# Optimization experiments

Hardware: AMD Instinct MI355X
Metric: run time of the kernel (lower is better)

Reference implementation:

```python
import jax, jax.numpy as jnp
import numpy as np

B, C, N, K, C_OUT = 16, 64, 2048, 3, 64


def setup_inputs() -> dict:
    key = jax.random.key(0)
    k1, k2, k3 = jax.random.split(key, 3)
    x = jax.random.normal(k1, (B, C, N), dtype=jnp.float32)
    # Conv1d params: weight [out_ch, in_ch, K], bias [out_ch]
    fan_in = C * K
    bound = 1.0 / np.sqrt(fan_in)
    W = jax.random.uniform(k2, (C_OUT, C, K), dtype=jnp.float32, minval=-bound, maxval=bound)
    b = jax.random.uniform(k3, (C_OUT,), dtype=jnp.float32, minval=-bound, maxval=bound)
    return {"x": x, "W": W, "b": b}


def reference(x, W, b):
    # x: [B, C, N]
    # pairwise squared-distance matrix over the length dim: [B, N, N]
    norm_sq = jnp.sum(x * x, axis=1, keepdims=True)              # [B, 1, N]
    dot = jnp.einsum('bcn,bcm->bnm', x, x)                       # [B, N, N]
    dist = norm_sq + jnp.swapaxes(norm_sq, 1, 2) - 2.0 * dot     # [B, N, N]
    # K smallest distances per point (self included, dist=0)
    _, idx = jax.lax.top_k(-dist, K)                             # [B, N, K]
    # gather neighbors: prime[b, c, n*K + k] = x[b, c, idx[b, n, k]]
    idx_flat = idx.reshape(B, 1, N * K)
    prime = jnp.take_along_axis(x, jnp.broadcast_to(idx_flat, (B, C, N * K)), axis=2)
    # Conv1d(kernel=K, stride=K, padding=0) -> [B, C_OUT, N]
    out = jax.lax.conv_general_dilated(
        prime, W, window_strides=(K,), padding='VALID',
        dimension_numbers=('NCH', 'OIH', 'NCH'))
    out = out + b[None, :, None]
    return jax.nn.relu(out)
```

## Files before the change

### kernel.cpp

```cpp
#include <hip/hip_runtime.h>
#include <float.h>

#define BB 16
#define CC 64
#define NN 2048
#define KNN 3
#define COUT 64
#define SPL 8

typedef _Float16 half8 __attribute__((ext_vector_type(8)));
typedef float f32x16 __attribute__((ext_vector_type(16)));

union u4h8 { uint4 v; half8 h; };

__device__ __forceinline__ void gl_lds16(const void* g, void* l) {
    __builtin_amdgcn_global_load_lds(
        (const __attribute__((address_space(1))) unsigned*)g,
        (__attribute__((address_space(3))) unsigned*)l, 16, 0, 0);
}

__global__ __launch_bounds__(256) void k_prep(const float* __restrict__ x,
                                              uint4* __restrict__ xe,
                                              unsigned* __restrict__ anc) {
    __shared__ float t[64][65];
    __shared__ float nsh[64];
    const int b = blockIdx.x;
    const int n0 = blockIdx.y * 64;
    const int tid = threadIdx.x;
    const int ln = tid & 63, g = tid >> 6;
#pragma unroll
    for (int i = 0; i < 16; ++i) {
        const int c = g + 4 * i;
        t[c][ln] = x[((size_t)b * CC + c) * NN + n0 + ln];
    }
    __syncthreads();
    if (tid < 64) {
        float s = 0.f;
#pragma unroll
        for (int c = 0; c < 64; ++c) s = fmaf(t[c][tid], t[c][tid], s);
        nsh[tid] = s;
    }
#pragma unroll
    for (int i = 0; i < 4; ++i) {
        const int cid = tid + 256 * i;
        const int lane = cid & 63;
        const int kblk = (cid >> 6) & 7;
        const int ctl = cid >> 9;
        const int m = ctl * 32 + (lane & 31);
        const int khalf = (lane >> 5) * 8;
        union { uint4 v; _Float16 h[8]; } pk;
#pragma unroll
        for (int j = 0; j < 8; ++j) {
            const int kg = kblk * 16 + khalf + j;
            const int ch = kg & 63;
            const float f = t[ch][m];
            const _Float16 hi = (_Float16)f;
            pk.h[j] = (kg < 64) ? hi : (_Float16)(f - (float)hi);
        }
        const int ct = (n0 >> 5) + ctl;
        xe[((size_t)(b * 64 + ct) * 8 + kblk) * 64 + lane] = pk.v;
    }
    __syncthreads();
    if (tid < 64) {
        const int ctl = tid >> 5, l = tid & 31;
        const int ct = (n0 >> 5) + ctl;
        const float h = -0.5f * nsh[ctl * 32 + l];
        const _Float16 a0 = (_Float16)h;
        const _Float16 a1 = (_Float16)(h - (float)a0);
        union { unsigned u; _Float16 hh[2]; } cu;
        cu.hh[0] = a0; cu.hh[1] = a1;
        anc[(size_t)(b * 64 + ct) * 32 + l] = cu.u;
    }
}

__global__ __launch_bounds__(256) void k_wprep(const float* __restrict__ W,
                                               uint4* __restrict__ Wf) {
    const int tid = threadIdx.x;
#pragma unroll
    for (int i = 0; i < 6; ++i) {
        const int id = tid + 256 * i;
        const int l = id & 63;
        const int kb = (id >> 6) & 3;
        const int ct2 = (id >> 8) & 1;
        const int kk = id >> 9;
        const int co = ct2 * 32 + (l & 31);
        union { uint4 v; _Float16 h[8]; } pk;
#pragma unroll
        for (int j = 0; j < 8; ++j) {
            const int c = kb * 16 + 8 * (l >> 5) + j;
            pk.h[j] = (_Float16)W[(co * CC + c) * KNN + kk];
        }
        Wf[id] = pk.v;
    }
}

__global__ __launch_bounds__(256, 4) void k_top3(const uint4* __restrict__ xe,
                                                 const unsigned* __restrict__ anc,
                                                 uint4* __restrict__ pk) {
    __shared__ uint4 buf[2][8][64];
    const int tid = threadIdx.x;
    const int lane = tid & 63;
    const int w = tid >> 6;
    const int wq = blockIdx.x * 4 + w;
    const int qgA = wq * 2, qgB = wq * 2 + 1;
    const int s = blockIdx.y;
    const int b = blockIdx.z;

    half8 bqA[8], bqB[8];
#pragma unroll
    for (int kb = 0; kb < 8; ++kb) {
        u4h8 tA, tB;
        tA.v = xe[((size_t)(b * 64 + qgA) * 8 + kb) * 64 + lane];
        tB.v = xe[((size_t)(b * 64 + qgB) * 8 + kb) * 64 + lane];
        bqA[kb] = tA.h; bqB[kb] = tB.h;
    }
    half8 bnc = {};
    if (lane < 32) { bnc[0] = (_Float16)1.0f; bnc[1] = (_Float16)1.0f; }

    float kA0 = -FLT_MAX, kA1 = -FLT_MAX, kA2 = -FLT_MAX;
    float kB0 = -FLT_MAX, kB1 = -FLT_MAX, kB2 = -FLT_MAX;
    int iA0 = -1, iA1 = -1, iA2 = -1;
    int iB0 = -1, iB1 = -1, iB2 = -1;
    const int hi4 = (lane >> 5) * 4;

    constexpr int TILES = NN / 32 / SPL;
    const int ct0 = s * TILES;
    const uint4* xb = xe + (size_t)(b * 64) * 512;
    const int kb0 = 2 * w, kb1 = 2 * w + 1;

    gl_lds16(xb + ((size_t)ct0 * 8 + kb0) * 64 + lane, &buf[0][kb0][0]);
    gl_lds16(xb + ((size_t)ct0 * 8 + kb1) * 64 + lane, &buf[0][kb1][0]);
    __syncthreads();

#pragma unroll
    for (int t = 0; t < TILES; ++t) {
        const int bi = t & 1;
        const int ct = ct0 + t;
        if (t + 1 < TILES) {
            gl_lds16(xb + ((size_t)(ct + 1) * 8 + kb0) * 64 + lane, &buf[bi ^ 1][kb0][0]);
            gl_lds16(xb + ((size_t)(ct + 1) * 8 + kb1) * 64 + lane, &buf[bi ^ 1][kb1][0]);
        }
        const unsigned av_u = anc[(size_t)(b * 64 + ct) * 32 + (lane & 31)];

        f32x16 accA = {}, accB = {};
        {
            u4h8 ah[4];
#pragma unroll
            for (int kb = 0; kb < 4; ++kb) ah[kb].v = buf[bi][kb][lane];
#pragma unroll
            for (int kb = 0; kb < 4; ++kb) {
                accA = __builtin_amdgcn_mfma_f32_32x32x16_f16(ah[kb].h, bqA[kb], accA, 0, 0, 0);
                accB = __builtin_amdgcn_mfma_f32_32x32x16_f16(ah[kb].h, bqB[kb], accB, 0, 0, 0);
            }
#pragma unroll
            for (int kb = 0; kb < 4; ++kb) {
                accA = __builtin_amdgcn_mfma_f32_32x32x16_f16(ah[kb].h, bqA[kb + 4], accA, 0, 0, 0);
                accB = __builtin_amdgcn_mfma_f32_32x32x16_f16(ah[kb].h, bqB[kb + 4], accB, 0, 0, 0);
            }
        }
        {
            u4h8 al[4];
#pragma unroll
            for (int kb = 0; kb < 4; ++kb) al[kb].v = buf[bi][4 + kb][lane];
#pragma unroll
            for (int kb = 0; kb < 4; ++kb) {
                accA = __builtin_amdgcn_mfma_f32_32x32x16_f16(al[kb].h, bqA[kb], accA, 0, 0, 0);
                accB = __builtin_amdgcn_mfma_f32_32x32x16_f16(al[kb].h, bqB[kb], accB, 0, 0, 0);
            }
            half8 av = {};
            union { unsigned u; _Float16 hh[2]; } cu;
            cu.u = av_u;
            av[0] = cu.hh[0]; av[1] = cu.hh[1];
            accA = __builtin_amdgcn_mfma_f32_32x32x16_f16(av, bnc, accA, 0, 0, 0);
            accB = __builtin_amdgcn_mfma_f32_32x32x16_f16(av, bnc, accB, 0, 0, 0);
        }

        const int mbase = t * 32 + hi4;
#pragma unroll
        for (int j = 0; j < 16; ++j) {
            const float a = accA[j];
            if (__any(a > kA2)) {
                const int m = mbase + (j & 3) + 8 * (j >> 2);
                const bool g0 = a > kA0, g1 = a > kA1, g2 = a > kA2;
                kA2 = g1 ? kA1 : (g2 ? a : kA2); iA2 = g1 ? iA1 : (g2 ? m : iA2);
                kA1 = g0 ? kA0 : (g1 ? a : kA1); iA1 = g0 ? iA0 : (g1 ? m : iA1);
                kA0 = g0 ? a : kA0;              iA0 = g0 ? m : iA0;
            }
        }
#pragma unroll
        for (int j = 0; j < 16; ++j) {
            const float a = accB[j];
            if (__any(a > kB2)) {
                const int m = mbase + (j & 3) + 8 * (j >> 2);
                const bool g0 = a > kB0, g1 = a > kB1, g2 = a > kB2;
                kB2 = g1 ? kB1 : (g2 ? a : kB2); iB2 = g1 ? iB1 : (g2 ? m : iB2);
                kB1 = g0 ? kB0 : (g1 ? a : kB1); iB1 = g0 ? iB0 : (g1 ? m : iB1);
                kB0 = g0 ? a : kB0;              iB0 = g0 ? m : iB0;
            }
        }
        __syncthreads();
    }

#pragma unroll
    for (int grp = 0; grp < 2; ++grp) {
        float K0 = grp ? kB0 : kA0, K1 = grp ? kB1 : kA1, K2 = grp ? kB2 : kA2;
        int I0 = grp ? iB0 : iA0, I1 = grp ? iB1 : iA1, I2 = grp ? iB2 : iA2;
        const float ok0 = __shfl_xor(K0, 32), ok1 = __shfl_xor(K1, 32), ok2 = __shfl_xor(K2, 32);
        const int oi0 = __shfl_xor(I0, 32), oi1 = __shfl_xor(I1, 32), oi2 = __shfl_xor(I2, 32);
        const float ck[3] = {ok0, ok1, ok2};
        const int cix[3] = {oi0, oi1, oi2};
#pragma unroll
        for (int r = 0; r < 3; ++r) {
            const float c = ck[r]; const int ci = cix[r];
            const bool b0 = (c > K0) || (c == K0 && ci < I0);
            const bool b1 = (c > K1) || (c == K1 && ci < I1);
            const bool b2 = (c > K2) || (c == K2 && ci < I2);
            K2 = b1 ? K1 : (b2 ? c : K2); I2 = b1 ? I1 : (b2 ? ci : I2);
            K1 = b0 ? K0 : (b1 ? c : K1); I1 = b0 ? I0 : (b1 ? ci : I1);
            K0 = b0 ? c : K0;             I0 = b0 ? ci : I0;
        }
        if (lane < 32) {
            const int q = (grp ? qgB : qgA) * 32 + lane;
            uint4 v;
            v.x = __float_as_uint(K0);
            v.y = __float_as_uint(K1);
            v.z = __float_as_uint(K2);
            v.w = (unsigned)I0 | ((unsigned)I1 << 8) | ((unsigned)I2 << 16);
            pk[((size_t)b * SPL + s) * NN + q] = v;
        }
    }
}

__global__ __launch_bounds__(256) void k_merge(const uint4* __restrict__ pk,
                                               int* __restrict__ fi) {
    const int t = blockIdx.x * 256 + threadIdx.x;
    if (t >= BB * NN) return;
    const int b = t / NN, n = t % NN;
    float dv[3 * SPL]; int iv[3 * SPL];
#pragma unroll
    for (int s = 0; s < SPL; ++s) {
        const uint4 v = pk[((size_t)b * SPL + s) * NN + n];
        dv[s * 3 + 0] = __uint_as_float(v.x);
        dv[s * 3 + 1] = __uint_as_float(v.y);
        dv[s * 3 + 2] = __uint_as_float(v.z);
        iv[s * 3 + 0] = (int)(v.w & 255u) + s * 256;
        iv[s * 3 + 1] = (int)((v.w >> 8) & 255u) + s * 256;
        iv[s * 3 + 2] = (int)((v.w >> 16) & 255u) + s * 256;
    }
    float bd = FLT_MAX; int bi = -1;
#pragma unroll
    for (int r = 0; r < 3; ++r) {
        float ck = -FLT_MAX; int ci = 0x7fffffff;
#pragma unroll
        for (int j = 0; j < 3 * SPL; ++j) {
            const bool after_prev = (dv[j] < bd) || (dv[j] == bd && iv[j] > bi);
            const bool better = (dv[j] > ck) || (dv[j] == ck && iv[j] < ci);
            if (after_prev && better) { ck = dv[j]; ci = iv[j]; }
        }
        fi[(size_t)t * 3 + r] = ci;
        bd = ck; bi = ci;
    }
}

__global__ __launch_bounds__(256) void k_conv(const uint4* __restrict__ xe,
                                              const uint4* __restrict__ Wf,
                                              const int* __restrict__ fi,
                                              const float* __restrict__ bias,
                                              float* __restrict__ out) {
    __shared__ float ot[64][65];
    const int b = blockIdx.y;
    const int n0 = blockIdx.x * 64;
    const int tid = threadIdx.x;
    const int l = tid & 63;
    const int w = tid >> 6;
    const int mt = w >> 1, ct2 = w & 1;
    const int p31 = l & 31, kh = l >> 5;
    const int npt = n0 + mt * 32 + p31;

    f32x16 acc = {};
    const uint4* xb = xe + (size_t)b * 64 * 8 * 64;
    const int fbase3 = (b * NN + npt) * KNN;
#pragma unroll
    for (int kk = 0; kk < KNN; ++kk) {
        const int src = fi[fbase3 + kk];
        const uint4* ap = xb + (size_t)(src >> 5) * 512 + (src & 31) + 32 * kh;
        uint4 af[4], bw[4];
#pragma unroll
        for (int kb = 0; kb < 4; ++kb) af[kb] = ap[(size_t)kb * 64];
#pragma unroll
        for (int kb = 0; kb < 4; ++kb) bw[kb] = Wf[((kk * 2 + ct2) * 4 + kb) * 64 + l];
#pragma unroll
        for (int kb = 0; kb < 4; ++kb) {
            u4h8 ua, ub;
            ua.v = af[kb]; ub.v = bw[kb];
            acc = __builtin_amdgcn_mfma_f32_32x32x16_f16(ua.h, ub.h, acc, 0, 0, 0);
        }
    }
    const int co = ct2 * 32 + p31;
    const float bv = bias[co];
#pragma unroll
    for (int j = 0; j < 16; ++j) {
        const int pt = mt * 32 + (j & 3) + 8 * (j >> 2) + 4 * kh;
        ot[co][pt] = fmaxf(acc[j] + bv, 0.f);
    }
    __syncthreads();
#pragma unroll
    for (int i = 0; i < 16; ++i) {
        const int v = tid + 256 * i;
        const int co2 = v >> 6, col = v & 63;
        out[((size_t)(b * COUT + co2)) * NN + n0 + col] = ot[co2][col];
    }
}

extern "C" void kernel_launch(void* const* d_in, const int* in_sizes, int n_in,
                              void* d_out, int out_size, void* d_ws, size_t ws_size,
                              hipStream_t stream) {
    const float* x = (const float*)d_in[0];
    const float* W = (const float*)d_in[1];
    const float* bias = (const float*)d_in[2];
    float* out = (float*)d_out;

    char* ws = (char*)d_ws;
    uint4* xe = (uint4*)(ws);
    unsigned* anc = (unsigned*)(ws + 8388608);
    uint4* Wf = (uint4*)(ws + 8519680);
    uint4* pk = (uint4*)(ws + 8544256);
    int* fi = (int*)(ws + 12738560);

    k_prep<<<dim3(BB, NN / 64), 256, 0, stream>>>(x, xe, anc);
    k_wprep<<<1, 256, 0, stream>>>(W, Wf);
    k_top3<<<dim3(8, SPL, BB), 256, 0, stream>>>(xe, anc, pk);
    k_merge<<<(BB * NN + 255) / 256, 256, 0, stream>>>(pk, fi);
    k_conv<<<dim3(NN / 64, BB), 256, 0, stream>>>(xe, Wf, fi, bias, out);
}
```

Measured before the change: 82.12 us.

## Preload whole split tile range into LDS once and drop per-tile barriers

```diff
diff --git a/kernel.cpp b/kernel.cpp
--- a/kernel.cpp
+++ b/kernel.cpp
@@ -94,17 +94,31 @@
     }
 }
 
-__global__ __launch_bounds__(256, 4) void k_top3(const uint4* __restrict__ xe,
+__global__ __launch_bounds__(256, 2) void k_top3(const uint4* __restrict__ xe,
                                                  const unsigned* __restrict__ anc,
                                                  uint4* __restrict__ pk) {
-    __shared__ uint4 buf[2][8][64];
+    __shared__ uint4 buf[4096];
+    const int bid = blockIdx.x;
+    const int s = bid & 7;
+    const int qgB8 = (bid >> 3) & 7;
+    const int b = bid >> 6;
+
     const int tid = threadIdx.x;
     const int lane = tid & 63;
     const int w = tid >> 6;
-    const int wq = blockIdx.x * 4 + w;
+    const int wq = qgB8 * 4 + w;
     const int qgA = wq * 2, qgB = wq * 2 + 1;
-    const int s = blockIdx.y;
-    const int b = blockIdx.z;
+
+    constexpr int TILES = NN / 32 / SPL;
+    const int ct0 = s * TILES;
+    const uint4* xb = xe + (size_t)(b * 64) * 512;
+
+    const uint4* gsrc = xb + (size_t)ct0 * 512;
+#pragma unroll
+    for (int i = 0; i < 16; ++i) {
+        const int c = w * 16 + i;
+        gl_lds16(gsrc + (size_t)c * 64 + lane, &buf[c * 64]);
+    }
 
     half8 bqA[8], bqB[8];
 #pragma unroll
@@ -114,6 +128,11 @@
         tB.v = xe[((size_t)(b * 64 + qgB) * 8 + kb) * 64 + lane];
         bqA[kb] = tA.h; bqB[kb] = tB.h;
     }
+    unsigned av_u[TILES];
+#pragma unroll
+    for (int t = 0; t < TILES; ++t)
+        av_u[t] = anc[(size_t)(b * 64 + ct0 + t) * 32 + (lane & 31)];
+
     half8 bnc = {};
     if (lane < 32) { bnc[0] = (_Float16)1.0f; bnc[1] = (_Float16)1.0f; }
 
@@ -123,30 +142,15 @@
     int iB0 = -1, iB1 = -1, iB2 = -1;
     const int hi4 = (lane >> 5) * 4;
 
-    constexpr int TILES = NN / 32 / SPL;
-    const int ct0 = s * TILES;
-    const uint4* xb = xe + (size_t)(b * 64) * 512;
-    const int kb0 = 2 * w, kb1 = 2 * w + 1;
-
-    gl_lds16(xb + ((size_t)ct0 * 8 + kb0) * 64 + lane, &buf[0][kb0][0]);
-    gl_lds16(xb + ((size_t)ct0 * 8 + kb1) * 64 + lane, &buf[0][kb1][0]);
     __syncthreads();
 
 #pragma unroll
     for (int t = 0; t < TILES; ++t) {
-        const int bi = t & 1;
-        const int ct = ct0 + t;
-        if (t + 1 < TILES) {
-            gl_lds16(xb + ((size_t)(ct + 1) * 8 + kb0) * 64 + lane, &buf[bi ^ 1][kb0][0]);
-            gl_lds16(xb + ((size_t)(ct + 1) * 8 + kb1) * 64 + lane, &buf[bi ^ 1][kb1][0]);
-        }
-        const unsigned av_u = anc[(size_t)(b * 64 + ct) * 32 + (lane & 31)];
-
         f32x16 accA = {}, accB = {};
         {
             u4h8 ah[4];
 #pragma unroll
-            for (int kb = 0; kb < 4; ++kb) ah[kb].v = buf[bi][kb][lane];
+            for (int kb = 0; kb < 4; ++kb) ah[kb].v = buf[(t * 8 + kb) * 64 + lane];
 #pragma unroll
             for (int kb = 0; kb < 4; ++kb) {
                 accA = __builtin_amdgcn_mfma_f32_32x32x16_f16(ah[kb].h, bqA[kb], accA, 0, 0, 0);
@@ -161,7 +165,7 @@
         {
             u4h8 al[4];
 #pragma unroll
-            for (int kb = 0; kb < 4; ++kb) al[kb].v = buf[bi][4 + kb][lane];
+            for (int kb = 0; kb < 4; ++kb) al[kb].v = buf[(t * 8 + 4 + kb) * 64 + lane];
 #pragma unroll
             for (int kb = 0; kb < 4; ++kb) {
                 accA = __builtin_amdgcn_mfma_f32_32x32x16_f16(al[kb].h, bqA[kb], accA, 0, 0, 0);
@@ -169,7 +173,7 @@
             }
             half8 av = {};
             union { unsigned u; _Float16 hh[2]; } cu;
-            cu.u = av_u;
+            cu.u = av_u[t];
             av[0] = cu.hh[0]; av[1] = cu.hh[1];
             accA = __builtin_amdgcn_mfma_f32_32x32x16_f16(av, bnc, accA, 0, 0, 0);
             accB = __builtin_amdgcn_mfma_f32_32x32x16_f16(av, bnc, accB, 0, 0, 0);
@@ -198,7 +202,6 @@
                 kB0 = g0 ? a : kB0;              iB0 = g0 ? m : iB0;
             }
         }
-        __syncthreads();
     }
 
 #pragma unroll
@@ -329,7 +332,7 @@
 
     k_prep<<<dim3(BB, NN / 64), 256, 0, stream>>>(x, xe, anc);
     k_wprep<<<1, 256, 0, stream>>>(W, Wf);
-    k_top3<<<dim3(8, SPL, BB), 256, 0, stream>>>(xe, anc, pk);
+    k_top3<<<dim3(BB * 8 * SPL), 256, 0, stream>>>(xe, anc, pk);
     k_merge<<<(BB * NN + 255) / 256, 256, 0, stream>>>(pk, fi);
     k_conv<<<dim3(NN / 64, BB), 256, 0, stream>>>(xe, Wf, fi, bias, out);
 }
```

Result: faster. 79.94 us (-2.7%).

## Restructure top-3 kernel: one query group per wave, 512-thread blocks, fewer splits

Applied to the files above, without the earlier changes.

```diff
diff --git a/kernel.cpp b/kernel.cpp
--- a/kernel.cpp
+++ b/kernel.cpp
@@ -6,7 +6,8 @@
 #define NN 2048
 #define KNN 3
 #define COUT 64
-#define SPL 8
+#define SPL 4
+#define TILES 16
 
 typedef _Float16 half8 __attribute__((ext_vector_type(8)));
 typedef float f32x16 __attribute__((ext_vector_type(16)));
@@ -94,140 +95,122 @@
     }
 }
 
-__global__ __launch_bounds__(256, 4) void k_top3(const uint4* __restrict__ xe,
+__global__ __launch_bounds__(512, 4) void k_top3(const uint4* __restrict__ xe,
                                                  const unsigned* __restrict__ anc,
                                                  uint4* __restrict__ pk) {
     __shared__ uint4 buf[2][8][64];
+    const int bid = blockIdx.x;
+    const int qb = bid >> 6;
+    const int rem = bid & 63;
+    const int b = rem >> 2;
+    const int s = rem & 3;
+
     const int tid = threadIdx.x;
     const int lane = tid & 63;
     const int w = tid >> 6;
-    const int wq = blockIdx.x * 4 + w;
-    const int qgA = wq * 2, qgB = wq * 2 + 1;
-    const int s = blockIdx.y;
-    const int b = blockIdx.z;
-
-    half8 bqA[8], bqB[8];
+    const int qg = qb * 8 + w;
+
+    const uint4* xb = xe + (size_t)(b * 64) * 512;
+    const int ct0 = s * TILES;
+
+    gl_lds16(xb + ((size_t)ct0 * 8 + w) * 64 + lane, &buf[0][w][0]);
+
+    half8 bq[8];
 #pragma unroll
     for (int kb = 0; kb < 8; ++kb) {
-        u4h8 tA, tB;
-        tA.v = xe[((size_t)(b * 64 + qgA) * 8 + kb) * 64 + lane];
-        tB.v = xe[((size_t)(b * 64 + qgB) * 8 + kb) * 64 + lane];
-        bqA[kb] = tA.h; bqB[kb] = tB.h;
-    }
+        u4h8 tq;
+        tq.v = xe[((size_t)(b * 64 + qg) * 8 + kb) * 64 + lane];
+        bq[kb] = tq.h;
+    }
+    unsigned av_u[TILES];
+#pragma unroll
+    for (int t = 0; t < TILES; ++t)
+        av_u[t] = anc[(size_t)(b * 64 + ct0 + t) * 32 + (lane & 31)];
+
     half8 bnc = {};
     if (lane < 32) { bnc[0] = (_Float16)1.0f; bnc[1] = (_Float16)1.0f; }
 
-    float kA0 = -FLT_MAX, kA1 = -FLT_MAX, kA2 = -FLT_MAX;
-    float kB0 = -FLT_MAX, kB1 = -FLT_MAX, kB2 = -FLT_MAX;
-    int iA0 = -1, iA1 = -1, iA2 = -1;
-    int iB0 = -1, iB1 = -1, iB2 = -1;
+    float k0 = -FLT_MAX, k1 = -FLT_MAX, k2 = -FLT_MAX;
+    int i0 = -1, i1 = -1, i2 = -1;
     const int hi4 = (lane >> 5) * 4;
 
-    constexpr int TILES = NN / 32 / SPL;
-    const int ct0 = s * TILES;
-    const uint4* xb = xe + (size_t)(b * 64) * 512;
-    const int kb0 = 2 * w, kb1 = 2 * w + 1;
-
-    gl_lds16(xb + ((size_t)ct0 * 8 + kb0) * 64 + lane, &buf[0][kb0][0]);
-    gl_lds16(xb + ((size_t)ct0 * 8 + kb1) * 64 + lane, &buf[0][kb1][0]);
     __syncthreads();
 
 #pragma unroll
     for (int t = 0; t < TILES; ++t) {
         const int bi = t & 1;
-        const int ct = ct0 + t;
-        if (t + 1 < TILES) {
-            gl_lds16(xb + ((size_t)(ct + 1) * 8 + kb0) * 64 + lane, &buf[bi ^ 1][kb0][0]);
-            gl_lds16(xb + ((size_t)(ct + 1) * 8 + kb1) * 64 + lane, &buf[bi ^ 1][kb1][0]);
-        }
-        const unsigned av_u = anc[(size_t)(b * 64 + ct) * 32 + (lane & 31)];
-
-        f32x16 accA = {}, accB = {};
+        if (t + 1 < TILES)
+            gl_lds16(xb + ((size_t)(ct0 + t + 1) * 8 + w) * 64 + lane,
+                     &buf[bi ^ 1][w][0]);
+
+        f32x16 acc = {};
         {
             u4h8 ah[4];
 #pragma unroll
             for (int kb = 0; kb < 4; ++kb) ah[kb].v = buf[bi][kb][lane];
 #pragma unroll
-            for (int kb = 0; kb < 4; ++kb) {
-                accA = __builtin_amdgcn_mfma_f32_32x32x16_f16(ah[kb].h, bqA[kb], accA, 0, 0, 0);
-                accB = __builtin_amdgcn_mfma_f32_32x32x16_f16(ah[kb].h, bqB[kb], accB, 0, 0, 0);
-            }
-#pragma unroll
-            for (int kb = 0; kb < 4; ++kb) {
-                accA = __builtin_amdgcn_mfma_f32_32x32x16_f16(ah[kb].h, bqA[kb + 4], accA, 0, 0, 0);
-                accB = __builtin_amdgcn_mfma_f32_32x32x16_f16(ah[kb].h, bqB[kb + 4], accB, 0, 0, 0);
-            }
+            for (int kb = 0; kb < 4; ++kb)
+                acc = __builtin_amdgcn_mfma_f32_32x32x16_f16(ah[kb].h, bq[kb], acc, 0, 0, 0);
+#pragma unroll
+            for (int kb = 0; kb < 4; ++kb)
+                acc = __builtin_amdgcn_mfma_f32_32x32x16_f16(ah[kb].h, bq[kb + 4], acc, 0, 0, 0);
         }
         {
             u4h8 al[4];
 #pragma unroll
             for (int kb = 0; kb < 4; ++kb) al[kb].v = buf[bi][4 + kb][lane];
 #pragma unroll
-            for (int kb = 0; kb < 4; ++kb) {
-                accA = __builtin_amdgcn_mfma_f32_32x32x16_f16(al[kb].h, bqA[kb], accA, 0, 0, 0);
-                accB = __builtin_amdgcn_mfma_f32_32x32x16_f16(al[kb].h, bqB[kb], accB, 0, 0, 0);
-            }
+            for (int kb = 0; kb < 4; ++kb)
+                acc = __builtin_amdgcn_mfma_f32_32x32x16_f16(al[kb].h, bq[kb], acc, 0, 0, 0);
             half8 av = {};
             union { unsigned u; _Float16 hh[2]; } cu;
-            cu.u = av_u;
+            cu.u = av_u[t];
             av[0] = cu.hh[0]; av[1] = cu.hh[1];
-            accA = __builtin_amdgcn_mfma_f32_32x32x16_f16(av, bnc, accA, 0, 0, 0);
-            accB = __builtin_amdgcn_mfma_f32_32x32x16_f16(av, bnc, accB, 0, 0, 0);
-        }
-
-        const int mbase = t * 32 + hi4;
-#pragma unroll
-        for (int j = 0; j < 16; ++j) {
-            const float a = accA[j];
-            if (__any(a > kA2)) {
-                const int m = mbase + (j & 3) + 8 * (j >> 2);
-                const bool g0 = a > kA0, g1 = a > kA1, g2 = a > kA2;
-                kA2 = g1 ? kA1 : (g2 ? a : kA2); iA2 = g1 ? iA1 : (g2 ? m : iA2);
-                kA1 = g0 ? kA0 : (g1 ? a : kA1); iA1 = g0 ? iA0 : (g1 ? m : iA1);
-                kA0 = g0 ? a : kA0;              iA0 = g0 ? m : iA0;
+            acc = __builtin_amdgcn_mfma_f32_32x32x16_f16(av, bnc, acc, 0, 0, 0);
+        }
+
+        float tmax = acc[0];
+#pragma unroll
+        for (int j = 1; j < 16; ++j) tmax = fmaxf(tmax, acc[j]);
+        if (__any(tmax > k2)) {
+            const int mbase = t * 32 + hi4;
+#pragma unroll
+            for (int j = 0; j < 16; ++j) {
+                const float a = acc[j];
+                if (__any(a > k2)) {
+                    const int m = mbase + (j & 3) + 8 * (j >> 2);
+                    const bool g0 = a > k0, g1 = a > k1, g2 = a > k2;
+                    k2 = g1 ? k1 : (g2 ? a : k2); i2 = g1 ? i1 : (g2 ? m : i2);
+                    k1 = g0 ? k0 : (g1 ? a : k1); i1 = g0 ? i0 : (g1 ? m : i1);
+                    k0 = g0 ? a : k0;             i0 = g0 ? m : i0;
+                }
             }
         }
-#pragma unroll
-        for (int j = 0; j < 16; ++j) {
-            const float a = accB[j];
-            if (__any(a > kB2)) {
-                const int m = mbase + (j & 3) + 8 * (j >> 2);
-                const bool g0 = a > kB0, g1 = a > kB1, g2 = a > kB2;
-                kB2 = g1 ? kB1 : (g2 ? a : kB2); iB2 = g1 ? iB1 : (g2 ? m : iB2);
-                kB1 = g0 ? kB0 : (g1 ? a : kB1); iB1 = g0 ? iB0 : (g1 ? m : iB1);
-                kB0 = g0 ? a : kB0;              iB0 = g0 ? m : iB0;
-            }
-        }
         __syncthreads();
     }
 
-#pragma unroll
-    for (int grp = 0; grp < 2; ++grp) {
-        float K0 = grp ? kB0 : kA0, K1 = grp ? kB1 : kA1, K2 = grp ? kB2 : kA2;
-        int I0 = grp ? iB0 : iA0, I1 = grp ? iB1 : iA1, I2 = grp ? iB2 : iA2;
-        const float ok0 = __shfl_xor(K0, 32), ok1 = __shfl_xor(K1, 32), ok2 = __shfl_xor(K2, 32);
-        const int oi0 = __shfl_xor(I0, 32), oi1 = __shfl_xor(I1, 32), oi2 = __shfl_xor(I2, 32);
-        const float ck[3] = {ok0, ok1, ok2};
-        const int cix[3] = {oi0, oi1, oi2};
-#pragma unroll
-        for (int r = 0; r < 3; ++r) {
-            const float c = ck[r]; const int ci = cix[r];
-            const bool b0 = (c > K0) || (c == K0 && ci < I0);
-            const bool b1 = (c > K1) || (c == K1 && ci < I1);
-            const bool b2 = (c > K2) || (c == K2 && ci < I2);
-            K2 = b1 ? K1 : (b2 ? c : K2); I2 = b1 ? I1 : (b2 ? ci : I2);
-            K1 = b0 ? K0 : (b1 ? c : K1); I1 = b0 ? I0 : (b1 ? ci : I1);
-            K0 = b0 ? c : K0;             I0 = b0 ? ci : I0;
-        }
-        if (lane < 32) {
-            const int q = (grp ? qgB : qgA) * 32 + lane;
-            uint4 v;
-            v.x = __float_as_uint(K0);
-            v.y = __float_as_uint(K1);
-            v.z = __float_as_uint(K2);
-            v.w = (unsigned)I0 | ((unsigned)I1 << 8) | ((unsigned)I2 << 16);
-            pk[((size_t)b * SPL + s) * NN + q] = v;
-        }
+    const float ok0 = __shfl_xor(k0, 32), ok1 = __shfl_xor(k1, 32), ok2 = __shfl_xor(k2, 32);
+    const int oi0 = __shfl_xor(i0, 32), oi1 = __shfl_xor(i1, 32), oi2 = __shfl_xor(i2, 32);
+    const float ck[3] = {ok0, ok1, ok2};
+    const int cix[3] = {oi0, oi1, oi2};
+#pragma unroll
+    for (int r = 0; r < 3; ++r) {
+        const float c = ck[r]; const int ci = cix[r];
+        const bool b0 = (c > k0) || (c == k0 && ci < i0);
+        const bool b1 = (c > k1) || (c == k1 && ci < i1);
+        const bool b2 = (c > k2) || (c == k2 && ci < i2);
+        k2 = b1 ? k1 : (b2 ? c : k2); i2 = b1 ? i1 : (b2 ? ci : i2);
+        k1 = b0 ? k0 : (b1 ? c : k1); i1 = b0 ? i0 : (b1 ? ci : i1);
+        k0 = b0 ? c : k0;             i0 = b0 ? ci : i0;
+    }
+    if (lane < 32) {
+        const int q = qg * 32 + lane;
+        uint4 v;
+        v.x = __float_as_uint(k0);
+        v.y = __float_as_uint(k1);
+        v.z = __float_as_uint(k2);
+        v.w = (unsigned)i0 | ((unsigned)i1 << 9) | ((unsigned)i2 << 18);
+        pk[((size_t)b * SPL + s) * NN + q] = v;
     }
 }
 
@@ -243,9 +226,9 @@
         dv[s * 3 + 0] = __uint_as_float(v.x);
         dv[s * 3 + 1] = __uint_as_float(v.y);
         dv[s * 3 + 2] = __uint_as_float(v.z);
-        iv[s * 3 + 0] = (int)(v.w & 255u) + s * 256;
-        iv[s * 3 + 1] = (int)((v.w >> 8) & 255u) + s * 256;
-        iv[s * 3 + 2] = (int)((v.w >> 16) & 255u) + s * 256;
+        iv[s * 3 + 0] = (int)(v.w & 511u) + s * 512;
+        iv[s * 3 + 1] = (int)((v.w >> 9) & 511u) + s * 512;
+        iv[s * 3 + 2] = (int)((v.w >> 18) & 511u) + s * 512;
     }
     float bd = FLT_MAX; int bi = -1;
 #pragma unroll
@@ -325,11 +308,11 @@
     unsigned* anc = (unsigned*)(ws + 8388608);
     uint4* Wf = (uint4*)(ws + 8519680);
     uint4* pk = (uint4*)(ws + 8544256);
-    int* fi = (int*)(ws + 12738560);
+    int* fi = (int*)(ws + 10641408);
 
     k_prep<<<dim3(BB, NN / 64), 256, 0, stream>>>(x, xe, anc);
     k_wprep<<<1, 256, 0, stream>>>(W, Wf);
-    k_top3<<<dim3(8, SPL, BB), 256, 0, stream>>>(xe, anc, pk);
+    k_top3<<<dim3(8 * 64), 512, 0, stream>>>(xe, anc, pk);
     k_merge<<<(BB * NN + 255) / 256, 256, 0, stream>>>(pk, fi);
     k_conv<<<dim3(NN / 64, BB), 256, 0, stream>>>(xe, Wf, fi, bias, out);
 }
```

After: 70.11 us. 14.6% less time.
